# Kernel optimization log

Hardware: AMD Instinct MI355X
Metric: run time of the kernel (lower is better)

Reference implementation:

```python
import jax, jax.numpy as jnp
import numpy as np

H, D = 12, 768
DH = D // H  # 64
B, S = 2, 2048


def setup_inputs() -> dict:
    key = jax.random.key(0)
    ks = jax.random.split(key, 9)
    scale = 1.0 / np.sqrt(D)
    x = jax.random.normal(ks[0], (B, S, D), dtype=jnp.float32)
    # per-head QKV linears stacked over heads: W* [H, D, DH], b* [H, DH]
    Wq = jax.random.normal(ks[1], (H, D, DH), dtype=jnp.float32) * scale
    Wk = jax.random.normal(ks[2], (H, D, DH), dtype=jnp.float32) * scale
    Wv = jax.random.normal(ks[3], (H, D, DH), dtype=jnp.float32) * scale
    bq = jax.random.normal(ks[4], (H, DH), dtype=jnp.float32) * scale
    bk = jax.random.normal(ks[5], (H, DH), dtype=jnp.float32) * scale
    bv = jax.random.normal(ks[6], (H, DH), dtype=jnp.float32) * scale
    Wo = jax.random.normal(ks[7], (D, D), dtype=jnp.float32) * scale
    bo = jax.random.normal(ks[8], (D,), dtype=jnp.float32) * scale
    return {"x": x, "Wq": Wq, "Wk": Wk, "Wv": Wv, "bq": bq, "bk": bk,
            "bv": bv, "Wo": Wo, "bo": bo, "c": 0}


def reference(x, Wq, Wk, Wv, bq, bk, bv, Wo, bo, c):
    # x: [B,S,D] -> q/k/v: [B,H,S,DH]  (vectorized over the per-head loop)
    q = jnp.einsum('bsd,hde->bhse', x, Wq) + bq[None, :, None, :]
    k = jnp.einsum('bsd,hde->bhse', x, Wk) + bk[None, :, None, :]
    v = jnp.einsum('bsd,hde->bhse', x, Wv) + bv[None, :, None, :]
    scores = jnp.einsum('bhse,bhte->bhst', q, k) / jnp.sqrt(jnp.float32(DH))
    probs = jax.nn.softmax(scores, axis=-1)  # [B,H,S,S]
    # c==1 noise branch and dropout are identity in eval / c==0 setting
    ctx = jnp.einsum('bhst,bhte->bhse', probs, v)  # [B,H,S,DH]
    # concat heads along last dim (head order == torch cat order)
    ctx = jnp.transpose(ctx, (0, 2, 1, 3)).reshape(B, S, D)
    out = ctx @ Wo + bo
    return out
```

## Files before the change

kernel.cpp:

```cpp
#include <hip/hip_runtime.h>
#include <hip/hip_bf16.h>
#include <math.h>

#define NH   12
#define DM   768
#define DH   64
#define NB   2
#define SEQ  2048

typedef short s8v  __attribute__((ext_vector_type(8)));
typedef short s4v  __attribute__((ext_vector_type(4)));
typedef float f32x4 __attribute__((ext_vector_type(4)));
typedef float f32x16 __attribute__((ext_vector_type(16)));
typedef s8v bfrag;

#define MFMA(a,b,c)   __builtin_amdgcn_mfma_f32_16x16x32_bf16(a,b,c,0,0,0)
#define MFMA32(a,b,c) __builtin_amdgcn_mfma_f32_32x32x16_bf16(a,b,c,0,0,0)

#define QSCALE 0.18033688011112042f

__device__ __forceinline__ short f2bf(float f) {
    __hip_bfloat16 h = __float2bfloat16(f);
    return *(short*)&h;
}
__device__ __forceinline__ float bf2f(short s) {
    __hip_bfloat16 h; *(short*)&h = s;
    return __bfloat162float(h);
}
__device__ __forceinline__ float fexp2(float x) { return __builtin_amdgcn_exp2f(x); }
__device__ __forceinline__ unsigned pkbf(float a, float b) {
    unsigned r;
    asm("v_cvt_pk_bf16_f32 %0, %1, %2" : "=v"(r) : "v"(a), "v"(b));
    return r;
}
__device__ __forceinline__ void pl32swap(unsigned &a, unsigned &b) {
    asm volatile("v_permlane32_swap_b32 %0, %1" : "+v"(a), "+v"(b));
}
__device__ __forceinline__ bfrag mkfrag(unsigned d0, unsigned d1, unsigned d2, unsigned d3) {
    union { unsigned u[4]; bfrag f; } X;
    X.u[0] = d0; X.u[1] = d1; X.u[2] = d2; X.u[3] = d3;
    return X.f;
}

__global__ __launch_bounds__(256) void prep_all(
    const float* __restrict__ x,
    const float* __restrict__ Wq, const float* __restrict__ Wk,
    const float* __restrict__ Wv, const float* __restrict__ Wo,
    short* __restrict__ xbf, short* __restrict__ Wt,
    short* __restrict__ Wot)
{
    const int bid = blockIdx.x;
    const int t = threadIdx.x;
    __shared__ __align__(16) short T0[64 * 72];

    if (bid < 1536) {
        const size_t gid = (size_t)bid * 256 + t;
        const float4 a = ((const float4*)x)[gid * 2];
        const float4 b = ((const float4*)x)[gid * 2 + 1];
        s8v o;
        o[0]=f2bf(a.x); o[1]=f2bf(a.y); o[2]=f2bf(a.z); o[3]=f2bf(a.w);
        o[4]=f2bf(b.x); o[5]=f2bf(b.y); o[6]=f2bf(b.z); o[7]=f2bf(b.w);
        *(s8v*)&xbf[gid * 8] = o;
    } else if (bid < 1968) {
        const int id = bid - 1536;
        const int dt = id % 12, mh = id / 12;
        const int mat = mh / NH, h = mh % NH;
        const float* W = (mat == 0 ? Wq : mat == 1 ? Wk : Wv) + (size_t)h * DM * DH;
        {
            const int r = t >> 2, e0 = (t & 3) * 16;
            #pragma unroll
            for (int q = 0; q < 4; ++q) {
                const float4 a = *(const float4*)&W[(size_t)(dt * 64 + r) * DH + e0 + q * 4];
                s4v s; s[0]=f2bf(a.x); s[1]=f2bf(a.y); s[2]=f2bf(a.z); s[3]=f2bf(a.w);
                *(s4v*)&T0[r * 72 + e0 + q * 4] = s;
            }
        }
        __syncthreads();
        {
            const int e = t >> 2, r0 = (t & 3) * 16;
            s8v s0, s1;
            #pragma unroll
            for (int i = 0; i < 8; ++i) { s0[i] = T0[(r0 + i) * 72 + e]; s1[i] = T0[(r0 + 8 + i) * 72 + e]; }
            short* dst = Wt + (size_t)mh * DH * DM + (size_t)e * DM + dt * 64 + r0;
            *(s8v*)&dst[0] = s0; *(s8v*)&dst[8] = s1;
        }
    } else {
        const int id = bid - 1968;
        const int ntl = id % 12, ktl = id / 12;
        {
            const int r = t >> 2, n0q = (t & 3) * 16;
            #pragma unroll
            for (int q = 0; q < 4; ++q) {
                const float4 a = *(const float4*)&Wo[(size_t)(ktl * 64 + r) * DM + ntl * 64 + n0q + q * 4];
                s4v s; s[0]=f2bf(a.x); s[1]=f2bf(a.y); s[2]=f2bf(a.z); s[3]=f2bf(a.w);
                *(s4v*)&T0[r * 72 + n0q + q * 4] = s;
            }
        }
        __syncthreads();
        {
            const int n = t >> 2, r0 = (t & 3) * 16;
            s8v h0, h1;
            #pragma unroll
            for (int i = 0; i < 8; ++i) {
                h0[i] = T0[(r0 + i) * 72 + n];
                h1[i] = T0[(r0 + 8 + i) * 72 + n];
            }
            const size_t off = (size_t)(ntl * 64 + n) * DM + ktl * 64 + r0;
            *(s8v*)&Wot[off] = h0; *(s8v*)&Wot[off + 8] = h1;
        }
    }
}

__global__ __launch_bounds__(256) void qkv_mfma(
    const short* __restrict__ xbf, const short* __restrict__ Wt,
    const float* __restrict__ bq, const float* __restrict__ bk,
    const float* __restrict__ bv,
    short* __restrict__ qo, short* __restrict__ ko, short* __restrict__ vto)
{
    const int mt = blockIdx.x, sp = blockIdx.y;
    const int slab0 = sp * 2;
    const int mat = slab0 / NH, h0 = slab0 % NH;
    __shared__ __align__(16) short Al[128 * 72];
    __shared__ __align__(16) short Bl[128 * 72];
    const int t = threadIdx.x;
    const int w = t >> 6, lane = t & 63, l15 = lane & 15, g = lane >> 4;
    const int m0 = mt * 128;
    const short* Ws = Wt + (size_t)slab0 * DH * DM;

    f32x4 acc[2][8];
    #pragma unroll
    for (int i = 0; i < 2; ++i)
        #pragma unroll
        for (int j = 0; j < 8; ++j) acc[i][j] = 0.f;

    for (int kt = 0; kt < DM / 64; ++kt) {
        const int k0 = kt * 64;
        {
            const int row = t >> 1, kc = (t & 1) * 32;
            #pragma unroll
            for (int q = 0; q < 4; ++q)
                *(s8v*)&Al[row * 72 + kc + q * 8] = *(const s8v*)&xbf[(size_t)(m0 + row) * DM + k0 + kc + q * 8];
            #pragma unroll
            for (int q = 0; q < 4; ++q)
                *(s8v*)&Bl[row * 72 + kc + q * 8] = *(const s8v*)&Ws[(size_t)row * DM + k0 + kc + q * 8];
        }
        __syncthreads();
        #pragma unroll
        for (int kk = 0; kk < 2; ++kk) {
            bfrag a[2], b[8];
            #pragma unroll
            for (int i = 0; i < 2; ++i) a[i] = *(const bfrag*)&Al[(w * 32 + 16 * i + l15) * 72 + kk * 32 + 8 * g];
            #pragma unroll
            for (int j = 0; j < 8; ++j) b[j] = *(const bfrag*)&Bl[(16 * j + l15) * 72 + kk * 32 + 8 * g];
            #pragma unroll
            for (int i = 0; i < 2; ++i)
                #pragma unroll
                for (int j = 0; j < 8; ++j) acc[i][j] = MFMA(a[i], b[j], acc[i][j]);
        }
        __syncthreads();
    }

    const float* bias0 = (mat == 0 ? bq : mat == 1 ? bk : bv);
    const float scl = (mat == 0) ? QSCALE : 1.0f;
    #pragma unroll
    for (int j = 0; j < 8; ++j) {
        const int h = h0 + (j >> 2);
        const int n = (j & 3) * 16 + l15;
        const float bia = bias0[h * DH + n];
        if (mat < 2) {
            short* out = (mat == 0 ? qo : ko);
            #pragma unroll
            for (int i = 0; i < 2; ++i)
                #pragma unroll
                for (int r = 0; r < 4; ++r) {
                    const int m = m0 + w * 32 + 16 * i + 4 * g + r;
                    const int bb = m >> 11, s = m & (SEQ - 1);
                    out[(((size_t)bb * NH + h) * SEQ + s) * DH + n] = f2bf((acc[i][j][r] + bia) * scl);
                }
        } else {
            #pragma unroll
            for (int i = 0; i < 2; ++i) {
                const int m = m0 + w * 32 + 16 * i + 4 * g;
                const int bb = m >> 11, s = m & (SEQ - 1);
                s4v sv;
                #pragma unroll
                for (int r = 0; r < 4; ++r) sv[r] = f2bf(acc[i][j][r] + bia);
                *(s4v*)&vto[(((size_t)bb * NH + h) * DH + n) * SEQ + s] = sv;
            }
        }
    }
}

__global__ __launch_bounds__(256, 4) void attn_mfma(
    const short* __restrict__ qg, const short* __restrict__ kg,
    const short* __restrict__ vtg, short* __restrict__ ctx)
{
    const int n_  = blockIdx.x;
    const int xcd = n_ & 7, s_ = n_ >> 3;
    const int bh = xcd * 3 + (s_ % 3);
    const int qb = s_ / 3;
    const int b = bh / NH, h = bh % NH;

    __shared__ __align__(16) float Cb[4][3][16][64];
    __shared__ float Ls[4][2][64];

    const int t = threadIdx.x;
    const int w = t >> 6, l = t & 63, lo = l & 31, hi = l >> 5;
    const size_t base  = (size_t)bh * SEQ * DH;
    const size_t vbase = (size_t)bh * DH * SEQ;
    const int qbase = qb * 64;

    bfrag qf[2][4];
    #pragma unroll
    for (int qt = 0; qt < 2; ++qt)
        #pragma unroll
        for (int esl = 0; esl < 4; ++esl)
            qf[qt][esl] = *(const bfrag*)&qg[base + (size_t)(qbase + qt * 32 + lo) * DH + esl * 16 + hi * 8];

    f32x16 o00, o01, o10, o11;
    o00 = 0.f; o01 = 0.f; o10 = 0.f; o11 = 0.f;
    float ls0 = 0.f, ls1 = 0.f;

    const short* kbase_p = kg + base;
    const short* vbase_p = vtg + vbase;
    const int r0 = w * 512;

    auto SMPV = [&](const f32x16& s0, const f32x16& s1,
                    const bfrag& vf00, const bfrag& vf01,
                    const bfrag& vf10, const bfrag& vf11) {
        float p0[16], p1[16];
        #pragma unroll
        for (int i = 0; i < 16; ++i) p0[i] = fexp2(s0[i]);
        #pragma unroll
        for (int i = 0; i < 16; ++i) p1[i] = fexp2(s1[i]);
        ls0 += ((p0[0]+p0[1])+(p0[2]+p0[3])) + ((p0[4]+p0[5])+(p0[6]+p0[7]))
             + ((p0[8]+p0[9])+(p0[10]+p0[11])) + ((p0[12]+p0[13])+(p0[14]+p0[15]));
        ls1 += ((p1[0]+p1[1])+(p1[2]+p1[3])) + ((p1[4]+p1[5])+(p1[6]+p1[7]))
             + ((p1[8]+p1[9])+(p1[10]+p1[11])) + ((p1[12]+p1[13])+(p1[14]+p1[15]));

        unsigned a0 = pkbf(p0[0],  p0[1]),  a1 = pkbf(p0[2],  p0[3]);
        unsigned a2 = pkbf(p0[4],  p0[5]),  a3 = pkbf(p0[6],  p0[7]);
        unsigned c0_ = pkbf(p0[8], p0[9]),  c1_ = pkbf(p0[10], p0[11]);
        unsigned c2_ = pkbf(p0[12], p0[13]), c3_ = pkbf(p0[14], p0[15]);
        pl32swap(a0, a2); pl32swap(a1, a3); pl32swap(c0_, c2_); pl32swap(c1_, c3_);
        const bfrag pa00 = mkfrag(a0, a1, a2, a3);
        const bfrag pa01 = mkfrag(c0_, c1_, c2_, c3_);

        unsigned d0 = pkbf(p1[0],  p1[1]),  d1 = pkbf(p1[2],  p1[3]);
        unsigned d2 = pkbf(p1[4],  p1[5]),  d3 = pkbf(p1[6],  p1[7]);
        unsigned e0_ = pkbf(p1[8], p1[9]),  e1_ = pkbf(p1[10], p1[11]);
        unsigned e2_ = pkbf(p1[12], p1[13]), e3_ = pkbf(p1[14], p1[15]);
        pl32swap(d0, d2); pl32swap(d1, d3); pl32swap(e0_, e2_); pl32swap(e1_, e3_);
        const bfrag pa10 = mkfrag(d0, d1, d2, d3);
        const bfrag pa11 = mkfrag(e0_, e1_, e2_, e3_);

        o00 = MFMA32(vf00, pa00, o00); o00 = MFMA32(vf01, pa01, o00);
        o10 = MFMA32(vf00, pa10, o10); o10 = MFMA32(vf01, pa11, o10);
        o01 = MFMA32(vf10, pa00, o01); o01 = MFMA32(vf11, pa01, o01);
        o11 = MFMA32(vf10, pa10, o11); o11 = MFMA32(vf11, pa11, o11);
    };

    bfrag kfA[4], kfB[4];
    bfrag vfA[4], vfB[4];
    #pragma unroll
    for (int esl = 0; esl < 4; ++esl)
        kfA[esl] = *(const bfrag*)&kbase_p[(size_t)(r0 + lo) * DH + esl * 16 + hi * 8];
    vfA[0] = *(const bfrag*)&vbase_p[(size_t)lo * SEQ + r0 + hi * 8];
    vfA[1] = *(const bfrag*)&vbase_p[(size_t)lo * SEQ + r0 + 16 + hi * 8];
    vfA[2] = *(const bfrag*)&vbase_p[(size_t)(32 + lo) * SEQ + r0 + hi * 8];
    vfA[3] = *(const bfrag*)&vbase_p[(size_t)(32 + lo) * SEQ + r0 + 16 + hi * 8];

    for (int it2 = 0; it2 < 8; ++it2) {
        {
            const int it = 2 * it2;
            f32x16 s0, s1; s0 = 0.f; s1 = 0.f;
            #pragma unroll
            for (int esl = 0; esl < 4; ++esl) {
                s0 = MFMA32(kfA[esl], qf[0][esl], s0);
                s1 = MFMA32(kfA[esl], qf[1][esl], s1);
            }
            {
                const short* kp = kbase_p + (size_t)(r0 + (it + 1) * 32 + lo) * DH;
                #pragma unroll
                for (int esl = 0; esl < 4; ++esl)
                    kfB[esl] = *(const bfrag*)&kp[esl * 16 + hi * 8];
                const int vc = r0 + (it + 1) * 32;
                vfB[0] = *(const bfrag*)&vbase_p[(size_t)lo * SEQ + vc + hi * 8];
                vfB[1] = *(const bfrag*)&vbase_p[(size_t)lo * SEQ + vc + 16 + hi * 8];
                vfB[2] = *(const bfrag*)&vbase_p[(size_t)(32 + lo) * SEQ + vc + hi * 8];
                vfB[3] = *(const bfrag*)&vbase_p[(size_t)(32 + lo) * SEQ + vc + 16 + hi * 8];
            }
            SMPV(s0, s1, vfA[0], vfA[1], vfA[2], vfA[3]);
        }
        {
            const int it = 2 * it2 + 1;
            f32x16 s0, s1; s0 = 0.f; s1 = 0.f;
            #pragma unroll
            for (int esl = 0; esl < 4; ++esl) {
                s0 = MFMA32(kfB[esl], qf[0][esl], s0);
                s1 = MFMA32(kfB[esl], qf[1][esl], s1);
            }
            if (it2 < 7) {
                const short* kp = kbase_p + (size_t)(r0 + (it + 1) * 32 + lo) * DH;
                #pragma unroll
                for (int esl = 0; esl < 4; ++esl)
                    kfA[esl] = *(const bfrag*)&kp[esl * 16 + hi * 8];
                const int vc = r0 + (it + 1) * 32;
                vfA[0] = *(const bfrag*)&vbase_p[(size_t)lo * SEQ + vc + hi * 8];
                vfA[1] = *(const bfrag*)&vbase_p[(size_t)lo * SEQ + vc + 16 + hi * 8];
                vfA[2] = *(const bfrag*)&vbase_p[(size_t)(32 + lo) * SEQ + vc + hi * 8];
                vfA[3] = *(const bfrag*)&vbase_p[(size_t)(32 + lo) * SEQ + vc + 16 + hi * 8];
            }
            SMPV(s0, s1, vfB[0], vfB[1], vfB[2], vfB[3]);
        }
    }

    Ls[w][0][l] = ls0;
    Ls[w][1][l] = ls1;
    #pragma unroll
    for (int c = 0; c < 4; ++c) {
        if (c == w) continue;
        const int idx = (w < c) ? w : w - 1;
        const f32x16 src = (c == 0) ? o00 : (c == 1) ? o01 : (c == 2) ? o10 : o11;
        #pragma unroll
        for (int r = 0; r < 16; ++r)
            Cb[c][idx][r][l] = src[r];
    }
    __syncthreads();

    f32x16 oc = (w == 0) ? o00 : (w == 1) ? o01 : (w == 2) ? o10 : o11;
    #pragma unroll
    for (int idx = 0; idx < 3; ++idx)
        #pragma unroll
        for (int r = 0; r < 16; ++r)
            oc[r] += Cb[w][idx][r][l];
    const int mqt = w >> 1, met = w & 1;
    float lt = 0.f;
    #pragma unroll
    for (int w2 = 0; w2 < 4; ++w2)
        lt += Ls[w2][mqt][lo] + Ls[w2][mqt][lo + 32];
    const float inv = 1.0f / lt;
    __syncthreads();

    unsigned* l2 = (unsigned*)&Cb[0][0][0][0];
    #pragma unroll
    for (int rq = 0; rq < 4; ++rq) {
        #pragma unroll
        for (int ph = 0; ph < 2; ++ph) {
            const int r = 4 * rq + 2 * ph;
            const int col = met * 16 + 2 * hi + 4 * rq + ph;
            l2[(mqt * 32 + lo) * 33 + col] = pkbf(oc[r] * inv, oc[r + 1] * inv);
        }
    }
    __syncthreads();

    {
        const int row = t >> 2, ch = (t & 3) * 8;
        short* crow = &ctx[((size_t)b * SEQ + qbase + row) * DM + h * DH];
        #pragma unroll
        for (int q = 0; q < 2; ++q) {
            uint4 u;
            u.x = l2[row * 33 + ch + q * 4 + 0];
            u.y = l2[row * 33 + ch + q * 4 + 1];
            u.z = l2[row * 33 + ch + q * 4 + 2];
            u.w = l2[row * 33 + ch + q * 4 + 3];
            *(uint4*)&crow[(ch + q * 4) * 2] = u;
        }
    }
}

__global__ __launch_bounds__(256) void out_mfma(
    const short* __restrict__ ctx,
    const short* __restrict__ Wot,
    const float* __restrict__ bo, float* __restrict__ out)
{
    const int mt = blockIdx.x, ntl = blockIdx.y;
    __shared__ __align__(16) short Al[128 * 72];
    __shared__ __align__(16) short Bh[64 * 72];
    const int t = threadIdx.x;
    const int w = t >> 6, lane = t & 63, l15 = lane & 15, g = lane >> 4;
    const int m0 = mt * 128, n0 = ntl * 64;

    f32x4 acc[2][4];
    #pragma unroll
    for (int i = 0; i < 2; ++i)
        #pragma unroll
        for (int j = 0; j < 4; ++j) acc[i][j] = 0.f;

    for (int kt = 0; kt < DM / 64; ++kt) {
        const int k0 = kt * 64;
        {
            const int row = t >> 1, kc = (t & 1) * 32;
            #pragma unroll
            for (int q = 0; q < 4; ++q)
                *(s8v*)&Al[row * 72 + kc + q * 8] = *(const s8v*)&ctx[(size_t)(m0 + row) * DM + k0 + kc + q * 8];
        }
        {
            const int n = t >> 2, kc = (t & 3) * 16;
            *(s8v*)&Bh[n * 72 + kc]     = *(const s8v*)&Wot[(size_t)(n0 + n) * DM + k0 + kc];
            *(s8v*)&Bh[n * 72 + kc + 8] = *(const s8v*)&Wot[(size_t)(n0 + n) * DM + k0 + kc + 8];
        }
        __syncthreads();
        #pragma unroll
        for (int kk = 0; kk < 2; ++kk) {
            bfrag ah[2];
            #pragma unroll
            for (int i = 0; i < 2; ++i)
                ah[i] = *(const bfrag*)&Al[(w * 32 + 16 * i + l15) * 72 + kk * 32 + 8 * g];
            #pragma unroll
            for (int j = 0; j < 4; ++j) {
                const bfrag bh_ = *(const bfrag*)&Bh[(16 * j + l15) * 72 + kk * 32 + 8 * g];
                #pragma unroll
                for (int i = 0; i < 2; ++i)
                    acc[i][j] = MFMA(ah[i], bh_, acc[i][j]);
            }
        }
        __syncthreads();
    }

    #pragma unroll
    for (int j = 0; j < 4; ++j) {
        const int n = n0 + 16 * j + l15;
        const float bia = bo[n];
        #pragma unroll
        for (int i = 0; i < 2; ++i)
            #pragma unroll
            for (int r = 0; r < 4; ++r) {
                const int m = m0 + w * 32 + 16 * i + 4 * g + r;
                out[(size_t)m * DM + n] = acc[i][j][r] + bia;
            }
    }
}

extern "C" void kernel_launch(void* const* d_in, const int* in_sizes, int n_in,
                              void* d_out, int out_size, void* d_ws, size_t ws_size,
                              hipStream_t stream) {
    const float* x  = (const float*)d_in[0];
    const float* Wq = (const float*)d_in[1];
    const float* Wk = (const float*)d_in[2];
    const float* Wv = (const float*)d_in[3];
    const float* bq = (const float*)d_in[4];
    const float* bk = (const float*)d_in[5];
    const float* bv = (const float*)d_in[6];
    const float* Wo = (const float*)d_in[7];
    const float* bo = (const float*)d_in[8];
    float* out = (float*)d_out;

    char* ws = (char*)d_ws;
    short* xbf   = (short*)(ws);
    short* Wt    = (short*)(ws + 6291456);
    short* Wot   = (short*)(ws + 9830400);
    short* qb    = (short*)(ws + 12189696);
    short* kb    = (short*)(ws + 18481152);
    short* vtb   = (short*)(ws + 31064064);
    short* ctx   = (short*)(ws + 37355520);

    prep_all<<<2112, 256, 0, stream>>>(x, Wq, Wk, Wv, Wo, xbf, Wt, Wot);
    qkv_mfma<<<dim3(32, 18), 256, 0, stream>>>(xbf, Wt, bq, bk, bv, qb, kb, vtb);
    attn_mfma<<<768, 256, 0, stream>>>(qb, kb, vtb, ctx);
    out_mfma<<<dim3(32, 12), 256, 0, stream>>>(ctx, Wot, bo, out);
}
```

Measured before the change: 111.2 us.

## Retile QKV GEMM to 64x192 blocks and raise MFMA wave priority in attention

The QKV projection kernel changes from 128x128 output tiles to 64-row by 192-column tiles (three head slabs per block). That raises the grid from 576 to 768 blocks to fill the GPU better and changes the A/B reuse ratio. Separately, the attention kernel wraps its MFMA bursts in s_setprio(1)/s_setprio(0) so waves issuing matrix ops get scheduling priority over waves doing loads and softmax. The new tiling reloads x more often per weight column and lowers MFMA reuse of the A fragment per wave.

```diff
diff --git a/kernel.cpp b/kernel.cpp
--- a/kernel.cpp
+++ b/kernel.cpp
@@ -118,44 +118,42 @@
     short* __restrict__ qo, short* __restrict__ ko, short* __restrict__ vto)
 {
     const int mt = blockIdx.x, sp = blockIdx.y;
-    const int slab0 = sp * 2;
+    const int slab0 = sp * 3;
     const int mat = slab0 / NH, h0 = slab0 % NH;
-    __shared__ __align__(16) short Al[128 * 72];
-    __shared__ __align__(16) short Bl[128 * 72];
+    __shared__ __align__(16) short Al[64 * 72];
+    __shared__ __align__(16) short Bl[192 * 72];
     const int t = threadIdx.x;
     const int w = t >> 6, lane = t & 63, l15 = lane & 15, g = lane >> 4;
-    const int m0 = mt * 128;
+    const int m0 = mt * 64;
     const short* Ws = Wt + (size_t)slab0 * DH * DM;
 
-    f32x4 acc[2][8];
-    #pragma unroll
-    for (int i = 0; i < 2; ++i)
-        #pragma unroll
-        for (int j = 0; j < 8; ++j) acc[i][j] = 0.f;
+    f32x4 acc[12];
+    #pragma unroll
+    for (int j = 0; j < 12; ++j) acc[j] = 0.f;
 
     for (int kt = 0; kt < DM / 64; ++kt) {
         const int k0 = kt * 64;
         {
-            const int row = t >> 1, kc = (t & 1) * 32;
-            #pragma unroll
-            for (int q = 0; q < 4; ++q)
-                *(s8v*)&Al[row * 72 + kc + q * 8] = *(const s8v*)&xbf[(size_t)(m0 + row) * DM + k0 + kc + q * 8];
-            #pragma unroll
-            for (int q = 0; q < 4; ++q)
-                *(s8v*)&Bl[row * 72 + kc + q * 8] = *(const s8v*)&Ws[(size_t)row * DM + k0 + kc + q * 8];
+            const int r = t >> 2, kc = (t & 3) * 16;
+            *(s8v*)&Al[r * 72 + kc]     = *(const s8v*)&xbf[(size_t)(m0 + r) * DM + k0 + kc];
+            *(s8v*)&Al[r * 72 + kc + 8] = *(const s8v*)&xbf[(size_t)(m0 + r) * DM + k0 + kc + 8];
+            #pragma unroll
+            for (int p = 0; p < 3; ++p) {
+                const int br = p * 64 + r;
+                *(s8v*)&Bl[br * 72 + kc]     = *(const s8v*)&Ws[(size_t)br * DM + k0 + kc];
+                *(s8v*)&Bl[br * 72 + kc + 8] = *(const s8v*)&Ws[(size_t)br * DM + k0 + kc + 8];
+            }
         }
         __syncthreads();
         #pragma unroll
         for (int kk = 0; kk < 2; ++kk) {
-            bfrag a[2], b[8];
-            #pragma unroll
-            for (int i = 0; i < 2; ++i) a[i] = *(const bfrag*)&Al[(w * 32 + 16 * i + l15) * 72 + kk * 32 + 8 * g];
-            #pragma unroll
-            for (int j = 0; j < 8; ++j) b[j] = *(const bfrag*)&Bl[(16 * j + l15) * 72 + kk * 32 + 8 * g];
-            #pragma unroll
-            for (int i = 0; i < 2; ++i)
-                #pragma unroll
-                for (int j = 0; j < 8; ++j) acc[i][j] = MFMA(a[i], b[j], acc[i][j]);
+            const bfrag a = *(const bfrag*)&Al[(w * 16 + l15) * 72 + kk * 32 + 8 * g];
+            bfrag b[12];
+            #pragma unroll
+            for (int j = 0; j < 12; ++j)
+                b[j] = *(const bfrag*)&Bl[(16 * j + l15) * 72 + kk * 32 + 8 * g];
+            #pragma unroll
+            for (int j = 0; j < 12; ++j) acc[j] = MFMA(a, b[j], acc[j]);
         }
         __syncthreads();
     }
@@ -163,30 +161,25 @@
     const float* bias0 = (mat == 0 ? bq : mat == 1 ? bk : bv);
     const float scl = (mat == 0) ? QSCALE : 1.0f;
     #pragma unroll
-    for (int j = 0; j < 8; ++j) {
+    for (int j = 0; j < 12; ++j) {
         const int h = h0 + (j >> 2);
         const int n = (j & 3) * 16 + l15;
         const float bia = bias0[h * DH + n];
         if (mat < 2) {
             short* out = (mat == 0 ? qo : ko);
             #pragma unroll
-            for (int i = 0; i < 2; ++i)
-                #pragma unroll
-                for (int r = 0; r < 4; ++r) {
-                    const int m = m0 + w * 32 + 16 * i + 4 * g + r;
-                    const int bb = m >> 11, s = m & (SEQ - 1);
-                    out[(((size_t)bb * NH + h) * SEQ + s) * DH + n] = f2bf((acc[i][j][r] + bia) * scl);
-                }
+            for (int r = 0; r < 4; ++r) {
+                const int m = m0 + w * 16 + 4 * g + r;
+                const int bb = m >> 11, s = m & (SEQ - 1);
+                out[(((size_t)bb * NH + h) * SEQ + s) * DH + n] = f2bf((acc[j][r] + bia) * scl);
+            }
         } else {
-            #pragma unroll
-            for (int i = 0; i < 2; ++i) {
-                const int m = m0 + w * 32 + 16 * i + 4 * g;
-                const int bb = m >> 11, s = m & (SEQ - 1);
-                s4v sv;
-                #pragma unroll
-                for (int r = 0; r < 4; ++r) sv[r] = f2bf(acc[i][j][r] + bia);
-                *(s4v*)&vto[(((size_t)bb * NH + h) * DH + n) * SEQ + s] = sv;
-            }
+            const int m = m0 + w * 16 + 4 * g;
+            const int bb = m >> 11, s = m & (SEQ - 1);
+            s4v sv;
+            #pragma unroll
+            for (int r = 0; r < 4; ++r) sv[r] = f2bf(acc[j][r] + bia);
+            *(s4v*)&vto[(((size_t)bb * NH + h) * DH + n) * SEQ + s] = sv;
         }
     }
 }
@@ -254,10 +247,12 @@
         const bfrag pa10 = mkfrag(d0, d1, d2, d3);
         const bfrag pa11 = mkfrag(e0_, e1_, e2_, e3_);
 
+        __builtin_amdgcn_s_setprio(1);
         o00 = MFMA32(vf00, pa00, o00); o00 = MFMA32(vf01, pa01, o00);
         o10 = MFMA32(vf00, pa10, o10); o10 = MFMA32(vf01, pa11, o10);
         o01 = MFMA32(vf10, pa00, o01); o01 = MFMA32(vf11, pa01, o01);
         o11 = MFMA32(vf10, pa10, o11); o11 = MFMA32(vf11, pa11, o11);
+        __builtin_amdgcn_s_setprio(0);
     };
 
     bfrag kfA[4], kfB[4];
@@ -274,11 +269,13 @@
         {
             const int it = 2 * it2;
             f32x16 s0, s1; s0 = 0.f; s1 = 0.f;
+            __builtin_amdgcn_s_setprio(1);
             #pragma unroll
             for (int esl = 0; esl < 4; ++esl) {
                 s0 = MFMA32(kfA[esl], qf[0][esl], s0);
                 s1 = MFMA32(kfA[esl], qf[1][esl], s1);
             }
+            __builtin_amdgcn_s_setprio(0);
             {
                 const short* kp = kbase_p + (size_t)(r0 + (it + 1) * 32 + lo) * DH;
                 #pragma unroll
@@ -295,11 +292,13 @@
         {
             const int it = 2 * it2 + 1;
             f32x16 s0, s1; s0 = 0.f; s1 = 0.f;
+            __builtin_amdgcn_s_setprio(1);
             #pragma unroll
             for (int esl = 0; esl < 4; ++esl) {
                 s0 = MFMA32(kfB[esl], qf[0][esl], s0);
                 s1 = MFMA32(kfB[esl], qf[1][esl], s1);
             }
+            __builtin_amdgcn_s_setprio(0);
             if (it2 < 7) {
                 const short* kp = kbase_p + (size_t)(r0 + (it + 1) * 32 + lo) * DH;
                 #pragma unroll
@@ -456,7 +455,7 @@
     short* ctx   = (short*)(ws + 37355520);
 
     prep_all<<<2112, 256, 0, stream>>>(x, Wq, Wk, Wv, Wo, xbf, Wt, Wot);
-    qkv_mfma<<<dim3(32, 18), 256, 0, stream>>>(xbf, Wt, bq, bk, bv, qb, kb, vtb);
+    qkv_mfma<<<dim3(64, 12), 256, 0, stream>>>(xbf, Wt, bq, bk, bv, qb, kb, vtb);
     attn_mfma<<<768, 256, 0, stream>>>(qb, kb, vtb, ctx);
     out_mfma<<<dim3(32, 12), 256, 0, stream>>>(ctx, Wot, bo, out);
 }
```

New measurement: 118.2 us. 1.06x slower.
